# Optimization experiments

Hardware: AMD Instinct MI355X
Metric: run time of the kernel (lower is better)

The kernel has to match this reference:

```python
import jax, jax.numpy as jnp
import numpy as np

E = 8          # num_experts
TOP_K = 2      # experts per token
D = 1024       # hidden_size
F = 2048       # intermediate_size
B, S = 2, 2048


def setup_inputs() -> dict:
    key = jax.random.key(0)
    k0, k1, k2, k3, k4 = jax.random.split(key, 5)
    return {
        "hidden_states": jax.random.normal(k0, (B, S, D), dtype=jnp.float32),
        "gate_w": jax.random.normal(k1, (D, E), dtype=jnp.float32) * 0.02,
        "w1": jax.random.normal(k2, (E, D, F), dtype=jnp.float32) * 0.02,
        "w2": jax.random.normal(k3, (E, F, D), dtype=jnp.float32) * 0.02,
        "w3": jax.random.normal(k4, (E, D, F), dtype=jnp.float32) * 0.02,
    }


def reference(hidden_states, gate_w, w1, w2, w3):
    b, s, d = hidden_states.shape
    x = hidden_states.reshape(-1, d)                       # [T, D]
    router_logits = x @ gate_w                             # [T, E]
    probs = jax.nn.softmax(router_logits, axis=-1)
    top_w, top_i = jax.lax.top_k(probs, TOP_K)             # [T, K]
    top_w = top_w / jnp.sum(top_w, axis=-1, keepdims=True)

    out = jnp.zeros_like(x)
    for e in range(E):
        # combine weight for expert e per token (0 if not routed here)
        w_e = jnp.sum(jnp.where(top_i == e, top_w, 0.0), axis=-1)   # [T]
        act = jax.nn.silu(x @ w1[e]) * (x @ w3[e])                  # [T, F]
        out = out + (act @ w2[e]) * w_e[:, None]
    return out.reshape(b, s, d)
```

## Files before the change

### kernel.cpp

```cpp
#include <hip/hip_runtime.h>

#define T_TOK 4096
#define D_DIM 1024
#define F_DIM 2048
#define E_NUM 8
#define MAX_TILES 136

typedef __attribute__((ext_vector_type(8))) short bf16x8;
typedef __attribute__((ext_vector_type(4))) float f32x4;
typedef unsigned short us;

__device__ __forceinline__ us f2bf(float f) {
  unsigned u = __builtin_bit_cast(unsigned, f);
  unsigned r = 0x7FFFu + ((u >> 16) & 1u);
  return (us)((u + r) >> 16);
}

__device__ __forceinline__ void gload16(const us* g, us* l) {
  __builtin_amdgcn_global_load_lds(
      (const __attribute__((address_space(1))) unsigned int*)g,
      (__attribute__((address_space(3))) unsigned int*)l, 16, 0, 0);
}

__device__ __forceinline__ f32x4 mfma16(bf16x8 a, bf16x8 b, f32x4 c) {
  return __builtin_amdgcn_mfma_f32_16x16x32_bf16(a, b, c, 0, 0, 0);
}

__global__ __launch_bounds__(256) void prep_kernel(
    const float* __restrict__ w1, const float* __restrict__ w3,
    const float* __restrict__ w2,
    us* __restrict__ W1t, us* __restrict__ W3t, us* __restrict__ W2t,
    const float* __restrict__ x, const float* __restrict__ gw,
    int* __restrict__ route_e, float2* __restrict__ route_w,
    us* __restrict__ Xb) {
  int z = blockIdx.z;
  int tid = threadIdx.x;

  if (z < 24) {
    __shared__ float tile[64][65];
    int which = z >> 3, e = z & 7;
    const float* src; us* dst; int M, N;
    if (which == 0)      { src = w1; dst = W1t; M = D_DIM; N = F_DIM; }
    else if (which == 1) { src = w3; dst = W3t; M = D_DIM; N = F_DIM; }
    else                 { src = w2; dst = W2t; M = F_DIM; N = D_DIM; }
    src += (size_t)e * M * N; dst += (size_t)e * M * N;
    int bid = blockIdx.y * gridDim.x + blockIdx.x;
    int nbx = N / 64;
    int i0 = (bid / nbx) * 64, j0 = (bid % nbx) * 64;
    int lr = tid >> 4, lc = (tid & 15) * 4;
    #pragma unroll
    for (int p = 0; p < 4; p++) {
      int row = p * 16 + lr;
      float4 v = *(const float4*)&src[(size_t)(i0 + row) * N + j0 + lc];
      tile[row][lc + 0] = v.x; tile[row][lc + 1] = v.y;
      tile[row][lc + 2] = v.z; tile[row][lc + 3] = v.w;
    }
    __syncthreads();
    #pragma unroll
    for (int p = 0; p < 4; p++) {
      int orow = p * 16 + lr;
      us b0 = f2bf(tile[lc + 0][orow]);
      us b1 = f2bf(tile[lc + 1][orow]);
      us b2 = f2bf(tile[lc + 2][orow]);
      us b3 = f2bf(tile[lc + 3][orow]);
      uint2 o;
      o.x = b0 | ((unsigned)b1 << 16);
      o.y = b2 | ((unsigned)b3 << 16);
      *(uint2*)&dst[(size_t)(j0 + orow) * M + i0 + lc] = o;
    }
  } else {
    int bid = (z - 24) * 512 + blockIdx.y * gridDim.x + blockIdx.x;
    int lane = tid & 63;
    int t = bid * 4 + (tid >> 6);
    float acc[E_NUM];
    #pragma unroll
    for (int e = 0; e < E_NUM; e++) acc[e] = 0.f;
    const float* xr = x + (size_t)t * D_DIM;
    us* xbr = Xb + (size_t)t * D_DIM;
    #pragma unroll
    for (int j = 0; j < D_DIM / 64; j++) {
      int d = lane + 64 * j;
      float xv = xr[d];
      xbr[d] = f2bf(xv);
      const float4* g = reinterpret_cast<const float4*>(gw + (size_t)d * E_NUM);
      float4 g0 = g[0], g1 = g[1];
      acc[0] += xv * g0.x; acc[1] += xv * g0.y; acc[2] += xv * g0.z; acc[3] += xv * g0.w;
      acc[4] += xv * g1.x; acc[5] += xv * g1.y; acc[6] += xv * g1.z; acc[7] += xv * g1.w;
    }
    #pragma unroll
    for (int e = 0; e < E_NUM; e++) {
      #pragma unroll
      for (int off = 32; off > 0; off >>= 1) acc[e] += __shfl_xor(acc[e], off);
    }
    if (lane == 0) {
      int e1 = 0; float l1 = acc[0];
      #pragma unroll
      for (int e = 1; e < E_NUM; e++) { if (acc[e] > l1) { l1 = acc[e]; e1 = e; } }
      int e2 = -1; float l2 = -1e30f;
      #pragma unroll
      for (int e = 0; e < E_NUM; e++) { if (e != e1 && acc[e] > l2) { l2 = acc[e]; e2 = e; } }
      float wa = 1.f / (1.f + expf(l2 - l1));
      float wb = 1.f / (1.f + expf(l1 - l2));
      route_e[t] = e1 | (e2 << 8);
      route_w[t] = make_float2(wa, wb);
    }
  }
}

__global__ __launch_bounds__(1024) void scatter_kernel(
    const int* __restrict__ route_e, const float2* __restrict__ route_w,
    int* __restrict__ counts, int4* __restrict__ tiles,
    int* __restrict__ list, float* __restrict__ wts) {
  int tid = threadIdx.x;
  int lane = tid & 63, wv = tid >> 6;
  __shared__ int wave_tot[16][E_NUM];
  __shared__ int wave_base[16][E_NUM];
  __shared__ int tot_s[E_NUM];

  int e_loc[8]; float w_loc[8];
  #pragma unroll
  for (int j = 0; j < 4; j++) {
    int t = tid * 4 + j;
    int re = route_e[t];
    float2 rw = route_w[t];
    e_loc[2 * j]     = re & 0xff; w_loc[2 * j]     = rw.x;
    e_loc[2 * j + 1] = re >> 8;   w_loc[2 * j + 1] = rw.y;
  }
  int c[E_NUM], pre[E_NUM];
  #pragma unroll
  for (int e = 0; e < E_NUM; e++) {
    int s = 0;
    #pragma unroll
    for (int j = 0; j < 8; j++) s += (e_loc[j] == e) ? 1 : 0;
    c[e] = s;
  }
  #pragma unroll
  for (int e = 0; e < E_NUM; e++) {
    int v = c[e];
    #pragma unroll
    for (int off = 1; off < 64; off <<= 1) {
      int u = __shfl_up(v, off);
      if (lane >= off) v += u;
    }
    pre[e] = v - c[e];
    if (lane == 63) wave_tot[wv][e] = v;
  }
  __syncthreads();
  if (tid < E_NUM) {
    int s = 0;
    for (int w = 0; w < 16; w++) { wave_base[w][tid] = s; s += wave_tot[w][tid]; }
    tot_s[tid] = s;
    counts[tid] = s;
  }
  __syncthreads();
  #pragma unroll
  for (int j = 0; j < 8; j++) {
    int e = e_loc[j];
    int off = 0;
    #pragma unroll
    for (int jj = 0; jj < 8; jj++)
      if (jj < j) off += (e_loc[jj] == e) ? 1 : 0;
    int basee = 0, pree = 0;
    #pragma unroll
    for (int ee = 0; ee < E_NUM; ee++)
      if (e == ee) { basee = wave_base[wv][ee]; pree = pre[ee]; }
    int pos = basee + pree + off;
    int t = tid * 4 + (j >> 1);
    list[e * T_TOK + pos] = t * 2 + (j & 1);
    wts[e * T_TOK + pos]  = w_loc[j];
  }
  if (tid < MAX_TILES) {
    int4 tt; tt.x = -1; tt.y = 0; tt.z = 0; tt.w = 0;
    int s = 0;
    #pragma unroll
    for (int e = 0; e < E_NUM; e++) {
      int ntl = (tot_s[e] + 63) >> 6;
      if (tid >= s && tid < s + ntl) { tt.x = e; tt.y = (tid - s) * 64; tt.z = tot_s[e]; }
      s += ntl;
    }
    tiles[tid] = tt;
  }
}

__global__ __launch_bounds__(256, 4) void gemm1_kernel(
    const us* __restrict__ Xb,
    const us* __restrict__ W1t,
    const us* __restrict__ W3t,
    const int4* __restrict__ tiles, const int* __restrict__ list,
    us* __restrict__ H) {
  __shared__ us As[64 * 64];
  __shared__ us B1s[64 * 64];
  __shared__ us B3s[64 * 64];
  __shared__ int rid_s[64];

  int4 td = tiles[blockIdx.y];
  int e = td.x;
  if (e < 0) return;
  int base = td.y, cnt = td.z;
  int nt = blockIdx.x;
  int tid = threadIdx.x;

  if (tid < 64) {
    int r = base + tid; if (r > cnt - 1) r = cnt - 1;
    rid_s[tid] = list[e * T_TOK + r];
  }
  __syncthreads();

  int lane = tid & 63, wid = tid >> 6;
  int sr = lane >> 3;
  int sg = (lane & 7) ^ sr;
  const us* a_src[2];
  #pragma unroll
  for (int t = 0; t < 2; t++)
    a_src[t] = Xb + (size_t)(rid_s[wid * 16 + t * 8 + sr] >> 1) * D_DIM + sg * 8;
  const us *b1_src[2], *b3_src[2];
  #pragma unroll
  for (int t = 0; t < 2; t++) {
    size_t row = (size_t)e * F_DIM + nt * 64 + wid * 16 + t * 8 + sr;
    b1_src[t] = W1t + row * D_DIM + sg * 8;
    b3_src[t] = W3t + row * D_DIM + sg * 8;
  }

  int wm = (wid >> 1) * 32, wn = (wid & 1) * 32;
  int frow = lane & 15;
  int fk = lane >> 4;

  unsigned offA[2][2], offB[2][2];
  #pragma unroll
  for (int mf = 0; mf < 2; mf++)
    #pragma unroll
    for (int kc = 0; kc < 2; kc++) {
      int m = wm + mf * 16 + frow, gk = kc * 4 + fk;
      offA[mf][kc] = m * 64 + ((gk ^ (m & 7)) * 8);
    }
  #pragma unroll
  for (int nf = 0; nf < 2; nf++)
    #pragma unroll
    for (int kc = 0; kc < 2; kc++) {
      int n = wn + nf * 16 + frow, gk = kc * 4 + fk;
      offB[nf][kc] = n * 64 + ((gk ^ (n & 7)) * 8);
    }

  f32x4 acc1[2][2], acc3[2][2];
  #pragma unroll
  for (int mf = 0; mf < 2; mf++)
    #pragma unroll
    for (int nf = 0; nf < 2; nf++) {
      f32x4 z = {0.f, 0.f, 0.f, 0.f};
      acc1[mf][nf] = z; acc3[mf][nf] = z;
    }

  #pragma unroll 1
  for (int k0 = 0; k0 < D_DIM; k0 += 64) {
    #pragma unroll
    for (int t = 0; t < 2; t++) {
      gload16(a_src[t] + k0, &As[(wid * 16 + t * 8) * 64]);
      gload16(b1_src[t] + k0, &B1s[(wid * 16 + t * 8) * 64]);
      gload16(b3_src[t] + k0, &B3s[(wid * 16 + t * 8) * 64]);
    }
    __syncthreads();
    #pragma unroll
    for (int kc = 0; kc < 2; kc++) {
      bf16x8 a[2], b1[2], b3[2];
      #pragma unroll
      for (int mf = 0; mf < 2; mf++) a[mf] = *(const bf16x8*)&As[offA[mf][kc]];
      #pragma unroll
      for (int nf = 0; nf < 2; nf++) {
        b1[nf] = *(const bf16x8*)&B1s[offB[nf][kc]];
        b3[nf] = *(const bf16x8*)&B3s[offB[nf][kc]];
      }
      #pragma unroll
      for (int mf = 0; mf < 2; mf++)
        #pragma unroll
        for (int nf = 0; nf < 2; nf++) {
          acc1[mf][nf] = mfma16(a[mf], b1[nf], acc1[mf][nf]);
          acc3[mf][nf] = mfma16(a[mf], b3[nf], acc3[mf][nf]);
        }
    }
    __syncthreads();
  }

  #pragma unroll
  for (int mf = 0; mf < 2; mf++) {
    #pragma unroll
    for (int i = 0; i < 4; i++) {
      int m = wm + mf * 16 + fk * 4 + i;
      if (base + m < cnt) {
        int rid = rid_s[m];
        us* hrow = H + (size_t)rid * F_DIM + nt * 64 + wn;
        #pragma unroll
        for (int nf = 0; nf < 2; nf++) {
          float z = acc1[mf][nf][i];
          float u = acc3[mf][nf][i];
          hrow[nf * 16 + frow] = f2bf((z / (1.f + expf(-z))) * u);
        }
      }
    }
  }
}

__global__ __launch_bounds__(256, 4) void gemm2_kernel(
    const us* __restrict__ H,
    const us* __restrict__ W2t,
    const int4* __restrict__ tiles, const int* __restrict__ list,
    const float* __restrict__ wts,
    float* __restrict__ out) {
  __shared__ us As[64 * 64];
  __shared__ us Bs[128 * 64];
  __shared__ int rid_s[64];
  __shared__ float wt_s[64];

  int4 td = tiles[blockIdx.y];
  int e = td.x;
  if (e < 0) return;
  int base = td.y, cnt = td.z;
  int nt = blockIdx.x;
  int tid = threadIdx.x;

  if (tid < 64) {
    int r = base + tid; if (r > cnt - 1) r = cnt - 1;
    rid_s[tid] = list[e * T_TOK + r];
    wt_s[tid] = wts[e * T_TOK + r];
  }
  __syncthreads();

  int lane = tid & 63, wid = tid >> 6;
  int sr = lane >> 3;
  int sg = (lane & 7) ^ sr;
  const us* a_src[2];
  #pragma unroll
  for (int t = 0; t < 2; t++)
    a_src[t] = H + (size_t)rid_s[wid * 16 + t * 8 + sr] * F_DIM + sg * 8;
  const us* b_src[4];
  #pragma unroll
  for (int t = 0; t < 4; t++)
    b_src[t] = W2t + ((size_t)e * D_DIM + nt * 128 + wid * 32 + t * 8 + sr) * F_DIM + sg * 8;

  int wm = (wid >> 1) * 32, wn = (wid & 1) * 64;
  int frow = lane & 15;
  int fk = lane >> 4;

  unsigned offA[2][2], offB[4][2];
  #pragma unroll
  for (int mf = 0; mf < 2; mf++)
    #pragma unroll
    for (int kc = 0; kc < 2; kc++) {
      int m = wm + mf * 16 + frow, gk = kc * 4 + fk;
      offA[mf][kc] = m * 64 + ((gk ^ (m & 7)) * 8);
    }
  #pragma unroll
  for (int nf = 0; nf < 4; nf++)
    #pragma unroll
    for (int kc = 0; kc < 2; kc++) {
      int n = wn + nf * 16 + frow, gk = kc * 4 + fk;
      offB[nf][kc] = n * 64 + ((gk ^ (n & 7)) * 8);
    }

  f32x4 acc[2][4];
  #pragma unroll
  for (int mf = 0; mf < 2; mf++)
    #pragma unroll
    for (int nf = 0; nf < 4; nf++) {
      f32x4 z = {0.f, 0.f, 0.f, 0.f};
      acc[mf][nf] = z;
    }

  #pragma unroll 1
  for (int k0 = 0; k0 < F_DIM; k0 += 64) {
    #pragma unroll
    for (int t = 0; t < 2; t++)
      gload16(a_src[t] + k0, &As[(wid * 16 + t * 8) * 64]);
    #pragma unroll
    for (int t = 0; t < 4; t++)
      gload16(b_src[t] + k0, &Bs[(wid * 32 + t * 8) * 64]);
    __syncthreads();
    #pragma unroll
    for (int kc = 0; kc < 2; kc++) {
      bf16x8 a[2], b[4];
      #pragma unroll
      for (int mf = 0; mf < 2; mf++) a[mf] = *(const bf16x8*)&As[offA[mf][kc]];
      #pragma unroll
      for (int nf = 0; nf < 4; nf++) b[nf] = *(const bf16x8*)&Bs[offB[nf][kc]];
      #pragma unroll
      for (int mf = 0; mf < 2; mf++)
        #pragma unroll
        for (int nf = 0; nf < 4; nf++)
          acc[mf][nf] = mfma16(a[mf], b[nf], acc[mf][nf]);
    }
    __syncthreads();
  }

  #pragma unroll
  for (int mf = 0; mf < 2; mf++) {
    #pragma unroll
    for (int i = 0; i < 4; i++) {
      int m = wm + mf * 16 + fk * 4 + i;
      if (base + m < cnt) {
        int tok = rid_s[m] >> 1;
        float w = wt_s[m];
        float* orow = out + (size_t)tok * D_DIM + nt * 128 + wn;
        #pragma unroll
        for (int nf = 0; nf < 4; nf++)
          atomicAdd(&orow[nf * 16 + frow], acc[mf][nf][i] * w);
      }
    }
  }
}

extern "C" void kernel_launch(void* const* d_in, const int* in_sizes, int n_in,
                              void* d_out, int out_size, void* d_ws, size_t ws_size,
                              hipStream_t stream) {
  const float* x  = (const float*)d_in[0];
  const float* gw = (const float*)d_in[1];
  const float* w1 = (const float*)d_in[2];
  const float* w2 = (const float*)d_in[3];
  const float* w3 = (const float*)d_in[4];
  float* out = (float*)d_out;

  char* ws = (char*)d_ws;
  const size_t LISTB = (size_t)E_NUM * T_TOK * 4;
  size_t o_counts  = 0;
  size_t o_tiles   = 256;
  size_t o_route_e = 4096;
  size_t o_route_w = o_route_e + (size_t)T_TOK * 4;
  size_t o_list    = o_route_w + (size_t)T_TOK * 8;
  size_t o_wts     = o_list + LISTB;
  size_t o_Xb      = o_wts + LISTB;
  size_t o_W1t     = o_Xb + (size_t)T_TOK * D_DIM * 2;
  size_t wt_sz     = (size_t)E_NUM * F_DIM * D_DIM * 2;
  size_t o_W3t     = o_W1t + wt_sz;
  size_t o_W2t     = o_W3t + wt_sz;
  size_t o_H       = o_W2t + wt_sz;

  int* counts    = (int*)(ws + o_counts);
  int4* tiles    = (int4*)(ws + o_tiles);
  int* route_e   = (int*)(ws + o_route_e);
  float2* route_w = (float2*)(ws + o_route_w);
  int* list      = (int*)(ws + o_list);
  float* wts     = (float*)(ws + o_wts);
  us* Xb  = (us*)(ws + o_Xb);
  us* W1t = (us*)(ws + o_W1t);
  us* W3t = (us*)(ws + o_W3t);
  us* W2t = (us*)(ws + o_W2t);
  us* H   = (us*)(ws + o_H);

  hipMemsetAsync(out, 0, (size_t)out_size * 4, stream);

  prep_kernel<<<dim3(32, 16, 26), 256, 0, stream>>>(
      w1, w3, w2, W1t, W3t, W2t, x, gw, route_e, route_w, Xb);

  scatter_kernel<<<dim3(1), 1024, 0, stream>>>(route_e, route_w, counts,
                                               tiles, list, wts);

  gemm1_kernel<<<dim3(F_DIM / 64, MAX_TILES), 256, 0, stream>>>(
      Xb, W1t, W3t, tiles, list, H);
  gemm2_kernel<<<dim3(D_DIM / 128, MAX_TILES), 256, 0, stream>>>(
      H, W2t, tiles, list, wts, out);
}
```

Measured before the change: 238.4 us.

## Move w2 transpose/convert from prep kernel into extra gemm1 blocks

```diff
diff --git a/kernel.cpp b/kernel.cpp
--- a/kernel.cpp
+++ b/kernel.cpp
@@ -5,6 +5,7 @@
 #define F_DIM 2048
 #define E_NUM 8
 #define MAX_TILES 136
+#define TZ 16
 
 typedef __attribute__((ext_vector_type(8))) short bf16x8;
 typedef __attribute__((ext_vector_type(4))) float f32x4;
@@ -28,30 +29,27 @@
 
 __global__ __launch_bounds__(256) void prep_kernel(
     const float* __restrict__ w1, const float* __restrict__ w3,
-    const float* __restrict__ w2,
-    us* __restrict__ W1t, us* __restrict__ W3t, us* __restrict__ W2t,
+    us* __restrict__ W1t, us* __restrict__ W3t,
     const float* __restrict__ x, const float* __restrict__ gw,
     int* __restrict__ route_e, float2* __restrict__ route_w,
     us* __restrict__ Xb) {
   int z = blockIdx.z;
   int tid = threadIdx.x;
 
-  if (z < 24) {
+  if (z < 16) {
     __shared__ float tile[64][65];
     int which = z >> 3, e = z & 7;
-    const float* src; us* dst; int M, N;
-    if (which == 0)      { src = w1; dst = W1t; M = D_DIM; N = F_DIM; }
-    else if (which == 1) { src = w3; dst = W3t; M = D_DIM; N = F_DIM; }
-    else                 { src = w2; dst = W2t; M = F_DIM; N = D_DIM; }
-    src += (size_t)e * M * N; dst += (size_t)e * M * N;
+    const float* src = (which == 0 ? w1 : w3);
+    us* dst = (which == 0 ? W1t : W3t);
+    src += (size_t)e * D_DIM * F_DIM; dst += (size_t)e * D_DIM * F_DIM;
     int bid = blockIdx.y * gridDim.x + blockIdx.x;
-    int nbx = N / 64;
+    int nbx = F_DIM / 64;
     int i0 = (bid / nbx) * 64, j0 = (bid % nbx) * 64;
     int lr = tid >> 4, lc = (tid & 15) * 4;
     #pragma unroll
     for (int p = 0; p < 4; p++) {
       int row = p * 16 + lr;
-      float4 v = *(const float4*)&src[(size_t)(i0 + row) * N + j0 + lc];
+      float4 v = *(const float4*)&src[(size_t)(i0 + row) * F_DIM + j0 + lc];
       tile[row][lc + 0] = v.x; tile[row][lc + 1] = v.y;
       tile[row][lc + 2] = v.z; tile[row][lc + 3] = v.w;
     }
@@ -66,10 +64,10 @@
       uint2 o;
       o.x = b0 | ((unsigned)b1 << 16);
       o.y = b2 | ((unsigned)b3 << 16);
-      *(uint2*)&dst[(size_t)(j0 + orow) * M + i0 + lc] = o;
+      *(uint2*)&dst[(size_t)(j0 + orow) * D_DIM + i0 + lc] = o;
     }
   } else {
-    int bid = (z - 24) * 512 + blockIdx.y * gridDim.x + blockIdx.x;
+    int bid = (z - 16) * 512 + blockIdx.y * gridDim.x + blockIdx.x;
     int lane = tid & 63;
     int t = bid * 4 + (tid >> 6);
     float acc[E_NUM];
@@ -187,18 +185,56 @@
     const us* __restrict__ W1t,
     const us* __restrict__ W3t,
     const int4* __restrict__ tiles, const int* __restrict__ list,
-    us* __restrict__ H) {
-  __shared__ us As[64 * 64];
-  __shared__ us B1s[64 * 64];
-  __shared__ us B3s[64 * 64];
+    us* __restrict__ H,
+    const float* __restrict__ w2, us* __restrict__ W2t) {
+  __shared__ __align__(16) us smem[3 * 64 * 64];
   __shared__ int rid_s[64];
-
-  int4 td = tiles[blockIdx.y];
+  int tid = threadIdx.x;
+
+  if (blockIdx.y < TZ) {
+    float (*tile)[65] = (float(*)[65])smem;
+    int slot = blockIdx.y * 32 + blockIdx.x;
+    int i0 = (slot >> 4) * 64;
+    int j0 = (slot & 15) * 64;
+    int lr = tid >> 4, lc = (tid & 15) * 4;
+    #pragma unroll 1
+    for (int e = 0; e < E_NUM; e++) {
+      const float* src = w2 + (size_t)e * F_DIM * D_DIM;
+      us* dst = W2t + (size_t)e * F_DIM * D_DIM;
+      #pragma unroll
+      for (int p = 0; p < 4; p++) {
+        int row = p * 16 + lr;
+        float4 v = *(const float4*)&src[(size_t)(i0 + row) * D_DIM + j0 + lc];
+        tile[row][lc + 0] = v.x; tile[row][lc + 1] = v.y;
+        tile[row][lc + 2] = v.z; tile[row][lc + 3] = v.w;
+      }
+      __syncthreads();
+      #pragma unroll
+      for (int p = 0; p < 4; p++) {
+        int orow = p * 16 + lr;
+        us b0 = f2bf(tile[lc + 0][orow]);
+        us b1 = f2bf(tile[lc + 1][orow]);
+        us b2 = f2bf(tile[lc + 2][orow]);
+        us b3 = f2bf(tile[lc + 3][orow]);
+        uint2 o;
+        o.x = b0 | ((unsigned)b1 << 16);
+        o.y = b2 | ((unsigned)b3 << 16);
+        *(uint2*)&dst[(size_t)(j0 + orow) * F_DIM + i0 + lc] = o;
+      }
+      __syncthreads();
+    }
+    return;
+  }
+
+  us* As  = smem;
+  us* B1s = smem + 4096;
+  us* B3s = smem + 8192;
+
+  int4 td = tiles[blockIdx.y - TZ];
   int e = td.x;
   if (e < 0) return;
   int base = td.y, cnt = td.z;
   int nt = blockIdx.x;
-  int tid = threadIdx.x;
 
   if (tid < 64) {
     int r = base + tid; if (r > cnt - 1) r = cnt - 1;
@@ -446,14 +482,14 @@
 
   hipMemsetAsync(out, 0, (size_t)out_size * 4, stream);
 
-  prep_kernel<<<dim3(32, 16, 26), 256, 0, stream>>>(
-      w1, w3, w2, W1t, W3t, W2t, x, gw, route_e, route_w, Xb);
+  prep_kernel<<<dim3(32, 16, 18), 256, 0, stream>>>(
+      w1, w3, W1t, W3t, x, gw, route_e, route_w, Xb);
 
   scatter_kernel<<<dim3(1), 1024, 0, stream>>>(route_e, route_w, counts,
                                                tiles, list, wts);
 
-  gemm1_kernel<<<dim3(F_DIM / 64, MAX_TILES), 256, 0, stream>>>(
-      Xb, W1t, W3t, tiles, list, H);
+  gemm1_kernel<<<dim3(F_DIM / 64, TZ + MAX_TILES), 256, 0, stream>>>(
+      Xb, W1t, W3t, tiles, list, H, w2, W2t);
   gemm2_kernel<<<dim3(D_DIM / 128, MAX_TILES), 256, 0, stream>>>(
       H, W2t, tiles, list, wts, out);
 }
```

Result: faster. 233.1 us (median of 2 runs) (-2.2%).
